# Optimization experiments

Hardware: AMD Instinct MI355X
Metric: run time of the kernel (lower is better)

Reference implementation:

```python
import jax, jax.numpy as jnp
import numpy as np

NEG_SLOPE = 0.1

def _mlp(x, W, b):
    # Linear + LeakyReLU(0.1), matching MLP(in, out, activation=LeakyReLU(0.1))
    return jax.nn.leaky_relu(jnp.einsum('bnc,cd->bnd', x, W) + b, negative_slope=NEG_SLOPE)

def setup_inputs() -> dict:
    key = jax.random.key(0)
    ks = jax.random.split(key, 5)
    B, N_down, N_up = 4, 16384, 65536
    C_down, C_up, C_out = 256, 128, 128
    x_down = jax.random.normal(ks[0], (B, N_down, C_down), dtype=jnp.float32)
    x_up = jax.random.normal(ks[1], (B, N_up, C_up), dtype=jnp.float32)
    up_idx = jax.random.randint(ks[2], (B, N_up, 1), 0, N_down, dtype=jnp.int64)
    W_lin = jax.random.normal(ks[3], (C_down, C_up), dtype=jnp.float32) * (1.0 / np.sqrt(C_down))
    b_lin = jnp.zeros((C_up,), dtype=jnp.float32)
    W_fus = jax.random.normal(ks[4], (2 * C_up, C_out), dtype=jnp.float32) * (1.0 / np.sqrt(2 * C_up))
    b_fus = jnp.zeros((C_out,), dtype=jnp.float32)
    return {"x_down": x_down, "x_up": x_up, "up_idx": up_idx,
            "W_lin": W_lin, "b_lin": b_lin, "W_fus": W_fus, "b_fus": b_fus}

def reference(x_down, x_up, up_idx, W_lin, b_lin, W_fus, b_fus):
    B, N_up, _ = up_idx.shape
    C_down = x_down.shape[-1]
    # upsampling: gather along point axis, index broadcast over channels
    idx = jnp.broadcast_to(up_idx, (B, N_up, C_down))
    x_g = jnp.take_along_axis(x_down, idx, axis=1)           # [B, N_up, C_down]
    x_lin = _mlp(x_g, W_lin, b_lin)                          # [B, N_up, C_up]
    x_cat = jnp.concatenate([x_up, x_lin], axis=-1)          # [B, N_up, 2*C_up]
    return _mlp(x_cat, W_fus, b_fus)                         # [B, N_up, C_out]
```

## Files before the change

kernel.cpp:

```cpp
#include <hip/hip_runtime.h>
#include <hip/hip_bf16.h>

constexpr int N_DOWN = 16384;
constexpr int N_UP   = 65536;
constexpr int BATCH  = 4;
constexpr int M_BLK  = 64;
constexpr int TS     = 264;

typedef __attribute__((ext_vector_type(8))) short short8;
typedef __attribute__((ext_vector_type(4))) float f32x4;

static __device__ inline unsigned short f2b(float f) {
  __hip_bfloat16 h = __float2bfloat16(f);
  return __builtin_bit_cast(unsigned short, h);
}
static __device__ inline void cvt_store4(__hip_bfloat16* dst, float4 v) {
  ushort4 s;
  s.x = f2b(v.x); s.y = f2b(v.y); s.z = f2b(v.z); s.w = f2b(v.w);
  *(ushort4*)dst = s;
}

__global__ void repack_w(const float* __restrict__ Wl,
                         const float* __restrict__ Wf,
                         __hip_bfloat16* __restrict__ pack) {
  int t = blockIdx.x * 256 + threadIdx.x;
  if (t >= 8192) return;
  int lane  = t & 63;
  int strip = (t >> 6) & 7;
  int kk    = (t >> 9) & 7;
  int w     = t >> 12;
  const float* W = w ? Wf : Wl;
  int q = lane >> 4;
  int l = lane & 15;
  int c = strip * 16 + l;
  short8 vals;
#pragma unroll
  for (int j = 0; j < 8; ++j) {
    int k = kk * 32 + q * 8 + j;
    vals[j] = (short)f2b(W[k * 128 + c]);
  }
  *(short8*)(pack + (size_t)t * 8) = vals;
}

__global__ __launch_bounds__(512, 6)
void fused_up(const float* __restrict__ x_down,
              const float* __restrict__ x_up,
              const int* __restrict__ up_idx,
              const float* __restrict__ b_lin,
              const float* __restrict__ b_fus,
              const __hip_bfloat16* __restrict__ pack,
              float* __restrict__ out) {
  __shared__ __hip_bfloat16 T[M_BLK * TS];

  const int tid  = threadIdx.x;
  const int wave = tid >> 6;
  const int lane = tid & 63;
  const int q    = lane >> 4;
  const int l    = lane & 15;

  const int m0 = blockIdx.x * M_BLK;
  const int b  = m0 >> 16;

  float4 xup[4];
#pragma unroll
  for (int j = 0; j < 4; ++j) {
    int f = j * 512 + tid;
    int r = f >> 5;
    int c4 = f & 31;
    xup[j] = *(const float4*)(x_up + (size_t)(m0 + r) * 128 + c4 * 4);
  }

  {
    const int lr = tid >> 3;
    const int s8 = tid & 7;
    const int gi = up_idx[m0 + lr];
    const float* src = x_down + ((size_t)b * N_DOWN + (size_t)gi) * 256;
    __hip_bfloat16* dst = T + lr * TS;
#pragma unroll
    for (int j = 0; j < 8; ++j) {
      int c4 = j * 8 + s8;
      float4 v = *(const float4*)(src + c4 * 4);
      cvt_store4(dst + c4 * 4, v);
    }
  }

  short8 B1[8];
#pragma unroll
  for (int kk = 0; kk < 8; ++kk)
    B1[kk] = *(const short8*)(pack + (size_t)((kk * 8 + wave) * 64 + lane) * 8);

  const float bias1 = b_lin[wave * 16 + l];
  const float bias2 = b_fus[wave * 16 + l];

  __syncthreads();

  f32x4 acc[4];
#pragma unroll
  for (int rg = 0; rg < 4; ++rg) acc[rg] = f32x4{0.f, 0.f, 0.f, 0.f};
#pragma unroll
  for (int kk = 0; kk < 8; ++kk) {
#pragma unroll
    for (int rg = 0; rg < 4; ++rg) {
      short8 a = *(const short8*)(T + (rg * 16 + l) * TS + kk * 32 + q * 8);
      acc[rg] = __builtin_amdgcn_mfma_f32_16x16x32_bf16(a, B1[kk], acc[rg], 0, 0, 0);
    }
  }
  __syncthreads();

#pragma unroll
  for (int j = 0; j < 4; ++j) {
    int f = j * 512 + tid;
    int r = f >> 5;
    int c4 = f & 31;
    cvt_store4(T + r * TS + c4 * 4, xup[j]);
  }
#pragma unroll
  for (int rg = 0; rg < 4; ++rg) {
#pragma unroll
    for (int i = 0; i < 4; ++i) {
      float v = acc[rg][i] + bias1;
      v = (v >= 0.f) ? v : 0.1f * v;
      T[(rg * 16 + q * 4 + i) * TS + 128 + wave * 16 + l] = __float2bfloat16(v);
    }
  }
  short8 B2[8];
#pragma unroll
  for (int kk = 0; kk < 8; ++kk)
    B2[kk] = *(const short8*)(pack + (size_t)(4096 + (kk * 8 + wave) * 64 + lane) * 8);

  __syncthreads();

  f32x4 acc2[4];
#pragma unroll
  for (int rg = 0; rg < 4; ++rg) acc2[rg] = f32x4{0.f, 0.f, 0.f, 0.f};
#pragma unroll
  for (int kk = 0; kk < 8; ++kk) {
#pragma unroll
    for (int rg = 0; rg < 4; ++rg) {
      short8 a = *(const short8*)(T + (rg * 16 + l) * TS + kk * 32 + q * 8);
      acc2[rg] = __builtin_amdgcn_mfma_f32_16x16x32_bf16(a, B2[kk], acc2[rg], 0, 0, 0);
    }
  }

#pragma unroll
  for (int rg = 0; rg < 4; ++rg) {
#pragma unroll
    for (int i = 0; i < 4; ++i) {
      float v = acc2[rg][i] + bias2;
      v = (v >= 0.f) ? v : 0.1f * v;
      out[(size_t)(m0 + rg * 16 + q * 4 + i) * 128 + wave * 16 + l] = v;
    }
  }
}

extern "C" void kernel_launch(void* const* d_in, const int* in_sizes, int n_in,
                              void* d_out, int out_size, void* d_ws, size_t ws_size,
                              hipStream_t stream) {
  const float* x_down = (const float*)d_in[0];
  const float* x_up   = (const float*)d_in[1];
  const int*   up_idx = (const int*)d_in[2];
  const float* W_lin  = (const float*)d_in[3];
  const float* b_lin  = (const float*)d_in[4];
  const float* W_fus  = (const float*)d_in[5];
  const float* b_fus  = (const float*)d_in[6];
  float* out = (float*)d_out;
  __hip_bfloat16* pack = (__hip_bfloat16*)d_ws;

  repack_w<<<32, 256, 0, stream>>>(W_lin, W_fus, pack);
  fused_up<<<(BATCH * N_UP) / M_BLK, 512, 0, stream>>>(
      x_down, x_up, up_idx, b_lin, b_fus, pack, out);
}
```

Baseline: 302.9 us.

## Apply first linear layer before gather to shrink work and traffic

After: 308.3 us. Within noise of the previous version (+1.8%).

```diff
diff --git a/kernel.cpp b/kernel.cpp
--- a/kernel.cpp
+++ b/kernel.cpp
@@ -42,14 +42,11 @@
   *(short8*)(pack + (size_t)t * 8) = vals;
 }
 
-__global__ __launch_bounds__(512, 6)
-void fused_up(const float* __restrict__ x_down,
-              const float* __restrict__ x_up,
-              const int* __restrict__ up_idx,
-              const float* __restrict__ b_lin,
-              const float* __restrict__ b_fus,
-              const __hip_bfloat16* __restrict__ pack,
-              float* __restrict__ out) {
+__global__ __launch_bounds__(512, 8)
+void mlp1_down(const float* __restrict__ x_down,
+               const float* __restrict__ b_lin,
+               const __hip_bfloat16* __restrict__ pack,
+               __hip_bfloat16* __restrict__ y) {
   __shared__ __hip_bfloat16 T[M_BLK * TS];
 
   const int tid  = threadIdx.x;
@@ -57,24 +54,12 @@
   const int lane = tid & 63;
   const int q    = lane >> 4;
   const int l    = lane & 15;
-
-  const int m0 = blockIdx.x * M_BLK;
-  const int b  = m0 >> 16;
-
-  float4 xup[4];
-#pragma unroll
-  for (int j = 0; j < 4; ++j) {
-    int f = j * 512 + tid;
-    int r = f >> 5;
-    int c4 = f & 31;
-    xup[j] = *(const float4*)(x_up + (size_t)(m0 + r) * 128 + c4 * 4);
-  }
+  const int m0   = blockIdx.x * M_BLK;
 
   {
     const int lr = tid >> 3;
     const int s8 = tid & 7;
-    const int gi = up_idx[m0 + lr];
-    const float* src = x_down + ((size_t)b * N_DOWN + (size_t)gi) * 256;
+    const float* src = x_down + (size_t)(m0 + lr) * 256;
     __hip_bfloat16* dst = T + lr * TS;
 #pragma unroll
     for (int j = 0; j < 8; ++j) {
@@ -88,9 +73,7 @@
 #pragma unroll
   for (int kk = 0; kk < 8; ++kk)
     B1[kk] = *(const short8*)(pack + (size_t)((kk * 8 + wave) * 64 + lane) * 8);
-
   const float bias1 = b_lin[wave * 16 + l];
-  const float bias2 = b_fus[wave * 16 + l];
 
   __syncthreads();
 
@@ -105,40 +88,71 @@
       acc[rg] = __builtin_amdgcn_mfma_f32_16x16x32_bf16(a, B1[kk], acc[rg], 0, 0, 0);
     }
   }
-  __syncthreads();
+
+#pragma unroll
+  for (int rg = 0; rg < 4; ++rg) {
+#pragma unroll
+    for (int i = 0; i < 4; ++i) {
+      float v = acc[rg][i] + bias1;
+      v = (v >= 0.f) ? v : 0.1f * v;
+      y[(size_t)(m0 + rg * 16 + q * 4 + i) * 128 + wave * 16 + l] = __float2bfloat16(v);
+    }
+  }
+}
+
+__global__ __launch_bounds__(512, 8)
+void fused_cat(const float* __restrict__ x_up,
+               const int* __restrict__ up_idx,
+               const __hip_bfloat16* __restrict__ y,
+               const float* __restrict__ b_fus,
+               const __hip_bfloat16* __restrict__ pack,
+               float* __restrict__ out) {
+  __shared__ __hip_bfloat16 T[M_BLK * TS];
+
+  const int tid  = threadIdx.x;
+  const int wave = tid >> 6;
+  const int lane = tid & 63;
+  const int q    = lane >> 4;
+  const int l    = lane & 15;
+  const int m0   = blockIdx.x * M_BLK;
+  const int b    = m0 >> 16;
+
+#pragma unroll
+  for (int j = 0; j < 2; ++j) {
+    int f = j * 512 + tid;
+    int r = f >> 4;
+    int c = f & 15;
+    int gi = up_idx[m0 + r];
+    const __hip_bfloat16* src = y + ((size_t)b * N_DOWN + gi) * 128 + c * 8;
+    *(short8*)(T + r * TS + 128 + c * 8) = *(const short8*)src;
+  }
 
 #pragma unroll
   for (int j = 0; j < 4; ++j) {
     int f = j * 512 + tid;
     int r = f >> 5;
     int c4 = f & 31;
-    cvt_store4(T + r * TS + c4 * 4, xup[j]);
+    float4 v = *(const float4*)(x_up + (size_t)(m0 + r) * 128 + c4 * 4);
+    cvt_store4(T + r * TS + c4 * 4, v);
   }
-#pragma unroll
-  for (int rg = 0; rg < 4; ++rg) {
-#pragma unroll
-    for (int i = 0; i < 4; ++i) {
-      float v = acc[rg][i] + bias1;
-      v = (v >= 0.f) ? v : 0.1f * v;
-      T[(rg * 16 + q * 4 + i) * TS + 128 + wave * 16 + l] = __float2bfloat16(v);
-    }
-  }
+
   short8 B2[8];
 #pragma unroll
   for (int kk = 0; kk < 8; ++kk)
     B2[kk] = *(const short8*)(pack + (size_t)(4096 + (kk * 8 + wave) * 64 + lane) * 8);
+  const float bias2 = b_fus[wave * 16 + l];
 
   __syncthreads();
 
-  f32x4 acc2[4];
+  f32x4 acc[4];
 #pragma unroll
-  for (int rg = 0; rg < 4; ++rg) acc2[rg] = f32x4{0.f, 0.f, 0.f, 0.f};
+  for (int rg = 0; rg < 4; ++rg) acc[rg] = f32x4{0.f, 0.f, 0.f, 0.f};
 #pragma unroll
   for (int kk = 0; kk < 8; ++kk) {
 #pragma unroll
     for (int rg = 0; rg < 4; ++rg) {
       short8 a = *(const short8*)(T + (rg * 16 + l) * TS + kk * 32 + q * 8);
-      acc2[rg] = __builtin_amdgcn_mfma_f32_16x16x32_bf16(a, B2[kk], acc2[rg], 0, 0, 0);
+      acc[rg] = __builtin_amdgcn_mfma_f32_16x16x32_bf16(a, B2[kk], acc[rg], 0, 0, 0);
     }
   }
 
@@ -146,7 +160,7 @@
   for (int rg = 0; rg < 4; ++rg) {
 #pragma unroll
     for (int i = 0; i < 4; ++i) {
-      float v = acc2[rg][i] + bias2;
+      float v = acc[rg][i] + bias2;
       v = (v >= 0.f) ? v : 0.1f * v;
       out[(size_t)(m0 + rg * 16 + q * 4 + i) * 128 + wave * 16 + l] = v;
     }
@@ -164,9 +178,11 @@
   const float* W_fus  = (const float*)d_in[5];
   const float* b_fus  = (const float*)d_in[6];
   float* out = (float*)d_out;
+
   __hip_bfloat16* pack = (__hip_bfloat16*)d_ws;
+  __hip_bfloat16* y    = (__hip_bfloat16*)((char*)d_ws + 131072);
 
   repack_w<<<32, 256, 0, stream>>>(W_lin, W_fus, pack);
-  fused_up<<<(BATCH * N_UP) / M_BLK, 512, 0, stream>>>(
-      x_down, x_up, up_idx, b_lin, b_fus, pack, out);
+  mlp1_down<<<(BATCH * N_DOWN) / M_BLK, 512, 0, stream>>>(x_down, b_lin, pack, y);
+  fused_cat<<<(BATCH * N_UP) / M_BLK, 512, 0, stream>>>(x_up, up_idx, y, b_fus, pack, out);
 }
```
